# Performance work log

Hardware: AMD Instinct MI355X
Metric: run time of the kernel (lower is better)

Reference implementation:

```python
import jax, jax.numpy as jnp
import numpy as np

B, S_LEN, H, NH, NT, NL, I = 8, 2048, 768, 12, 32, 9, 3072
SPAN = 64
NSP = S_LEN // SPAN
TAG_RATE = 2
DH = H // NH
EPS = 1e-12


def rope(x):
    # interleaved-pair rotary position embedding, x: [B, L, H]
    L = x.shape[1]
    half = x.shape[2] // 2
    inv = 1.0 / (10000.0 ** (jnp.arange(half, dtype=jnp.float32) / half))
    ang = jnp.arange(L, dtype=jnp.float32)[:, None] * inv[None, :]  # [L, half]
    sin, cos = jnp.sin(ang), jnp.cos(ang)
    x2 = x.reshape(x.shape[0], L, half, 2)
    xe, xo = x2[..., 0], x2[..., 1]
    return jnp.stack([xe * cos - xo * sin, xe * sin + xo * cos], axis=-1).reshape(x.shape)


def layernorm(x, g, b):
    m = jnp.mean(x, axis=-1, keepdims=True)
    v = jnp.mean((x - m) ** 2, axis=-1, keepdims=True)
    return (x - m) * jax.lax.rsqrt(v + EPS) * g + b


def mha(q_in, kv_in, Wqkv, bqkv, Wo, bo):
    # torch nn.MultiheadAttention math (eval), batched over leading span axis
    Wq, Wk, Wv = jnp.split(Wqkv, 3, axis=0)
    bq, bk, bv = jnp.split(bqkv, 3)
    def heads(x, W, b):
        return (x @ W.T + b).reshape(x.shape[0], x.shape[1], NH, DH)
    q = heads(q_in, Wq, bq)
    k = heads(kv_in, Wk, bk)
    v = heads(kv_in, Wv, bv)
    scores = jnp.einsum('nqhd,nkhd->nhqk', q, k) * (1.0 / DH ** 0.5)
    a = jax.nn.softmax(scores, axis=-1)
    o = jnp.einsum('nhqk,nkhd->nqhd', a, v).reshape(q_in.shape[0], q_in.shape[1], H)
    return o @ Wo.T + bo


def setup_inputs() -> dict:
    key = jax.random.key(0)
    ks = jax.random.split(key, 16)
    p = lambda i, shape: (0.02 * jax.random.normal(ks[i], shape)).astype(jnp.float32)
    inp = {}
    inp['word_embedding'] = jax.random.normal(ks[0], (B, S_LEN, H), dtype=jnp.float32)
    # fixed-length, non-overlapping spans covering the sequence
    inp['span_starts'] = jnp.broadcast_to(jnp.arange(NSP, dtype=jnp.int32) * SPAN, (B, NSP))
    inp['span_tags'] = jax.random.randint(ks[1], (B, NSP), 0, NT)
    inp['tag_emb'] = p(2, (NT, H))
    inp['sa_Wqkv'] = p(3, (3 * H, H)); inp['sa_bqkv'] = jnp.zeros((3 * H,), jnp.float32)
    inp['sa_Wo'] = p(4, (H, H)); inp['sa_bo'] = jnp.zeros((H,), jnp.float32)
    inp['at_Wqkv'] = p(5, (3 * H, H)); inp['at_bqkv'] = jnp.zeros((3 * H,), jnp.float32)
    inp['at_Wo'] = p(6, (H, H)); inp['at_bo'] = jnp.zeros((H,), jnp.float32)
    inp['an_g'] = jnp.ones((H,), jnp.float32); inp['an_b'] = jnp.zeros((H,), jnp.float32)
    inp['W1'] = p(7, (I, H)); inp['b1'] = jnp.zeros((I,), jnp.float32)
    inp['W2'] = p(8, (H, I)); inp['b2'] = jnp.zeros((H,), jnp.float32)
    inp['fn_g'] = jnp.ones((H,), jnp.float32); inp['fn_b'] = jnp.zeros((H,), jnp.float32)
    inp['Wout'] = p(9, (NL, H)); inp['bout'] = jnp.zeros((NL,), jnp.float32)
    return inp


def reference(word_embedding, span_starts, span_tags, tag_emb,
              sa_Wqkv, sa_bqkv, sa_Wo, sa_bo,
              at_Wqkv, at_bqkv, at_Wo, at_bo,
              an_g, an_b, W1, b1, W2, b2, fn_g, fn_b, Wout, bout):
    raw = word_embedding  # hidden dropout p=0 (eval) -> identity
    xe = rope(word_embedding)
    # pack all spans: [B, NSP*SPAN] token positions
    pos = (span_starts[..., None] + jnp.arange(SPAN)).reshape(B, NSP * SPAN)
    spans = jnp.take_along_axis(xe, pos[..., None], axis=1).reshape(B * NSP, SPAN, H)
    # if_add_a_self_attention: X += self_attention(X, X, X)
    X = spans + mha(spans, spans, sa_Wqkv, sa_bqkv, sa_Wo, sa_bo)
    # enumerate_mode == 'self_attention': prepend tag embedding token, self-attend, drop it
    tagv = tag_emb[span_tags.reshape(-1)][:, None, :]  # [B*NSP, 1, H]
    qkv = jnp.concatenate([tagv, X], axis=1)           # [B*NSP, SPAN+1, H]
    res = mha(qkv, qkv, at_Wqkv, at_bqkv, at_Wo, at_bo)[:, 1:, :]
    # scatter-add results back into the full sequence
    taged = jnp.zeros_like(word_embedding).at[jnp.arange(B)[:, None], pos].add(
        res.reshape(B, NSP * SPAN, H))
    # if_merge_by_add branch
    out_emb = layernorm(raw + taged * TAG_RATE, an_g, an_b)
    ff = jax.nn.relu(out_emb @ W1.T + b1) @ W2.T + b2
    out = layernorm(ff + out_emb, fn_g, fn_b)
    return out @ Wout.T + bout
```

## Files before the change

### kernel.cpp

```cpp
#include <hip/hip_runtime.h>


typedef __attribute__((ext_vector_type(8))) short short8;
typedef __attribute__((ext_vector_type(4))) float f32x4;

typedef const __attribute__((address_space(1))) unsigned int* gas1_t;
typedef __attribute__((address_space(3))) unsigned int* las3_t;

#define DEVI static __device__ __forceinline__
#define VMCNT(n) asm volatile("s_waitcnt vmcnt(" #n ")" ::: "memory")

DEVI void gload_lds16(const void* g, void* l){
  __builtin_amdgcn_global_load_lds((gas1_t)g, (las3_t)l, 16, 0, 0);
}

DEVI unsigned short f2bf(float f){
  union { float f; unsigned u; } v; v.f = f;
  unsigned u = v.u;
  return (unsigned short)((u + 0x7fffu + ((u >> 16) & 1u)) >> 16);
}
DEVI float bf2f(unsigned short h){
  union { unsigned u; float f; } v; v.u = ((unsigned)h) << 16; return v.f;
}

__global__ void k_ropetab(float2* __restrict__ tab){
  int idx = blockIdx.x * 256 + threadIdx.x;
  if (idx >= 2048 * 384) return;
  int l = idx / 384, i = idx % 384;
  float inv = __expf(-(float)i * (9.210340371976184f / 384.0f));
  float ang = (float)l * inv;
  tab[idx] = make_float2(cosf(ang), sinf(ang));
}

__global__ void k_f2bf(const float* __restrict__ src, unsigned short* __restrict__ dst, int n){
  int i = blockIdx.x * 256 + threadIdx.x;
  if (i * 4 >= n) return;
  float4 v = *(const float4*)(src + (size_t)i * 4);
  ushort4 o;
  o.x = f2bf(v.x); o.y = f2bf(v.y); o.z = f2bf(v.z); o.w = f2bf(v.w);
  *(ushort4*)(dst + (size_t)i * 4) = o;
}

__global__ void k_gather_rope(const float* __restrict__ we, const int* __restrict__ starts,
                              const float2* __restrict__ tab, unsigned short* __restrict__ spans){
  int idx = blockIdx.x * 256 + threadIdx.x;
  int r  = idx / 192;
  int c4 = idx % 192;
  int span = r >> 6, s = r & 63;
  int b = span >> 5;
  int l = starts[span] + s;
  float4 x = *(const float4*)(we + ((size_t)b * 2048 + l) * 768 + c4 * 4);
  int i0 = c4 * 2;
  float2 cs0 = tab[l * 384 + i0];
  float2 cs1 = tab[l * 384 + i0 + 1];
  ushort4 o;
  o.x = f2bf(x.x * cs0.x - x.y * cs0.y);
  o.y = f2bf(x.x * cs0.y + x.y * cs0.x);
  o.z = f2bf(x.z * cs1.x - x.w * cs1.y);
  o.w = f2bf(x.z * cs1.y + x.w * cs1.x);
  *(ushort4*)(spans + (size_t)r * 768 + c4 * 4) = o;
}

__global__ void k_fill_tag(const float* __restrict__ tag_emb, const int* __restrict__ tags,
                           unsigned short* __restrict__ at_in){
  int span = blockIdx.x;
  int tag = tags[span];
  const float* src = tag_emb + (size_t)tag * 768;
  unsigned short* dst = at_in + (size_t)span * 65 * 768;
  for (int j = threadIdx.x; j < 768; j += 256) dst[j] = f2bf(src[j]);
}

template<int EPI>
__global__ __launch_bounds__(512, 2)
void k_gemm256(const unsigned short* __restrict__ A, const unsigned short* __restrict__ Bw,
               const float* __restrict__ bias, void* __restrict__ outp,
               const unsigned short* __restrict__ resid, int M, int N, int K, int nbx)
{
  __shared__ unsigned short Asl[4 * 256 * 32];
  __shared__ unsigned short Bsl[4 * 256 * 32];
  const int t0 = threadIdx.x;
  const int w = t0 >> 6, lane = t0 & 63;
  const int g = lane >> 4, li = lane & 15;
  const int wm = w >> 2, wn = w & 3;

  const int nwg = gridDim.x;
  const int bid = blockIdx.x;
  const int q = nwg >> 3, r8 = nwg & 7;
  const int xcd = bid & 7, off = bid >> 3;
  const int swz = (xcd < r8 ? xcd * (q + 1) : r8 * (q + 1) + (xcd - r8) * q) + off;
  const int m0 = (swz / nbx) * 256, n0 = (swz % nbx) * 256;

  const int srow = lane >> 2;
  const int sgc = (((lane & 3) ^ ((lane >> 3) & 3)) << 3);
  const int cs = ((g ^ ((li >> 1) & 3)) << 3);

  f32x4 acc[8][4];
  #pragma unroll
  for (int i = 0; i < 8; i++)
    #pragma unroll
    for (int j = 0; j < 4; j++) acc[i][j] = f32x4{0.f, 0.f, 0.f, 0.f};

  const int KT = K >> 5;

  #define STAGE(t_, s_) do { \
    const unsigned short* ga0 = A  + (size_t)(m0 +       w*16 + srow) * K + (t_)*32 + sgc; \
    const unsigned short* ga1 = A  + (size_t)(m0 + 128 + w*16 + srow) * K + (t_)*32 + sgc; \
    const unsigned short* gb0 = Bw + (size_t)(n0 +       w*16 + srow) * K + (t_)*32 + sgc; \
    const unsigned short* gb1 = Bw + (size_t)(n0 + 128 + w*16 + srow) * K + (t_)*32 + sgc; \
    gload_lds16(ga0, Asl + (s_)*8192 + (      w*16)*32); \
    gload_lds16(ga1, Asl + (s_)*8192 + (128 + w*16)*32); \
    gload_lds16(gb0, Bsl + (s_)*8192 + (      w*16)*32); \
    gload_lds16(gb1, Bsl + (s_)*8192 + (128 + w*16)*32); \
  } while(0)

  STAGE(0, 0);
  STAGE(1, 1);
  VMCNT(4);
  __builtin_amdgcn_s_barrier();

  for (int t = 0; t < KT; ++t){
    const int slot = t & 3;
    const unsigned short* As = Asl + slot * 8192;
    const unsigned short* Bs = Bsl + slot * 8192;

    short8 af[8], bfr[4];
    #pragma unroll
    for (int m = 0; m < 8; m++)
      af[m] = *(const short8*)(As + (wm * 128 + m * 16 + li) * 32 + cs);
    #pragma unroll
    for (int n = 0; n < 4; n++)
      bfr[n] = *(const short8*)(Bs + (wn * 64 + n * 16 + li) * 32 + cs);

    if (t + 2 < KT) STAGE(t + 2, (t + 2) & 3);

    #pragma unroll
    for (int m = 0; m < 8; m++)
      #pragma unroll
      for (int n = 0; n < 4; n++)
        acc[m][n] = __builtin_amdgcn_mfma_f32_16x16x32_bf16(af[m], bfr[n], acc[m][n], 0, 0, 0);

    if (t + 1 < KT){
      __builtin_amdgcn_sched_barrier(0);
      if (t + 2 < KT) { VMCNT(4); } else { VMCNT(0); }
      __builtin_amdgcn_s_barrier();
    }
  }
  #undef STAGE

  unsigned short* outb = (unsigned short*)outp;
  float* outf = (float*)outp;
  #pragma unroll
  for (int m = 0; m < 8; m++){
    const int row = m0 + wm * 128 + m * 16 + g * 4;
    #pragma unroll
    for (int n = 0; n < 4; n++){
      const int col = n0 + wn * 64 + n * 16 + li;
      const float bv = bias[col];
      #pragma unroll
      for (int r = 0; r < 4; r++){
        float v = acc[m][n][r] + bv;
        const int orow = row + r;
        if (EPI == 1) v += bf2f(resid[(size_t)orow * N + col]);
        if (EPI == 3) v = v > 0.f ? v : 0.f;
        if (EPI == 2){
          outf[(size_t)orow * N + col] = v;
        } else if (EPI == 1){
          outb[(size_t)(orow + orow / 64 + 1) * N + col] = f2bf(v);
        } else {
          outb[(size_t)orow * N + col] = f2bf(v);
        }
      }
    }
  }
}

template<int AT>
__global__ __launch_bounds__(64)
void k_attn(const unsigned short* __restrict__ qkv, unsigned short* __restrict__ outp)
{
  constexpr int Lkv  = AT ? 65 : 64;
  constexpr int qoff = AT ? 1 : 0;
  constexpr int NKF  = AT ? 5 : 4;
  constexpr int VK   = AT ? 65 : 64;
  constexpr int KKPV = AT ? 3 : 2;
  const int h = blockIdx.x;
  const int span = blockIdx.y;
  const int base = span * Lkv;
  const int lane = threadIdx.x;
  const int g = lane >> 4, li = lane & 15;

  __shared__ unsigned short P[64 * 104];
  if (AT){
    #pragma unroll
    for (int j = 0; j < 16; j++) P[lane * 104 + 80 + j] = 0;
  }

  short8 qf[4][2];
  #pragma unroll
  for (int m = 0; m < 4; m++)
    #pragma unroll
    for (int kq = 0; kq < 2; kq++)
      qf[m][kq] = *(const short8*)(qkv + (size_t)(base + qoff + m * 16 + li) * 2304 + h * 64 + kq * 32 + g * 8);

  f32x4 sc[4][NKF];
  #pragma unroll
  for (int m = 0; m < 4; m++)
    #pragma unroll
    for (int n = 0; n < NKF; n++) sc[m][n] = f32x4{0.f, 0.f, 0.f, 0.f};

  #pragma unroll
  for (int kq = 0; kq < 2; kq++){
    #pragma unroll
    for (int n = 0; n < NKF; n++){
      int krow = n * 16 + li; if (krow >= Lkv) krow = Lkv - 1;
      short8 kf = *(const short8*)(qkv + (size_t)(base + krow) * 2304 + 768 + h * 64 + kq * 32 + g * 8);
      #pragma unroll
      for (int m = 0; m < 4; m++)
        sc[m][n] = __builtin_amdgcn_mfma_f32_16x16x32_bf16(qf[m][kq], kf, sc[m][n], 0, 0, 0);
    }
  }

  const float scale = 0.125f;
  #pragma unroll
  for (int m = 0; m < 4; m++){
    #pragma unroll
    for (int r = 0; r < 4; r++){
      float mx = -1e30f;
      #pragma unroll
      for (int n = 0; n < NKF; n++){
        float v = sc[m][n][r] * scale;
        if (n * 16 + li >= VK) v = -1e30f;
        sc[m][n][r] = v;
        mx = fmaxf(mx, v);
      }
      mx = fmaxf(mx, __shfl_xor(mx, 1, 64));
      mx = fmaxf(mx, __shfl_xor(mx, 2, 64));
      mx = fmaxf(mx, __shfl_xor(mx, 4, 64));
      mx = fmaxf(mx, __shfl_xor(mx, 8, 64));
      float sum = 0.f;
      #pragma unroll
      for (int n = 0; n < NKF; n++){
        float p = __expf(sc[m][n][r] - mx);
        sc[m][n][r] = p;
        sum += p;
      }
      sum += __shfl_xor(sum, 1, 64);
      sum += __shfl_xor(sum, 2, 64);
      sum += __shfl_xor(sum, 4, 64);
      sum += __shfl_xor(sum, 8, 64);
      const float inv = 1.f / sum;
      const int prow = m * 16 + g * 4 + r;
      #pragma unroll
      for (int n = 0; n < NKF; n++)
        P[prow * 104 + n * 16 + li] = f2bf(sc[m][n][r] * inv);
    }
  }
  __syncthreads();

  f32x4 oacc[4][4];
  #pragma unroll
  for (int m = 0; m < 4; m++)
    #pragma unroll
    for (int n = 0; n < 4; n++) oacc[m][n] = f32x4{0.f, 0.f, 0.f, 0.f};

  #pragma unroll
  for (int kp = 0; kp < KKPV; kp++){
    short8 pf[4];
    #pragma unroll
    for (int m = 0; m < 4; m++)
      pf[m] = *(const short8*)(P + (m * 16 + li) * 104 + kp * 32 + g * 8);
    #pragma unroll
    for (int n = 0; n < 4; n++){
      short8 vf;
      #pragma unroll
      for (int i = 0; i < 8; i++){
        int k = kp * 32 + g * 8 + i;
        unsigned short vv = 0;
        if (k < VK) vv = qkv[(size_t)(base + k) * 2304 + 1536 + h * 64 + n * 16 + li];
        vf[i] = (short)vv;
      }
      #pragma unroll
      for (int m = 0; m < 4; m++)
        oacc[m][n] = __builtin_amdgcn_mfma_f32_16x16x32_bf16(pf[m], vf, oacc[m][n], 0, 0, 0);
    }
  }

  #pragma unroll
  for (int m = 0; m < 4; m++)
    #pragma unroll
    for (int n = 0; n < 4; n++)
      #pragma unroll
      for (int r = 0; r < 4; r++){
        int q = m * 16 + g * 4 + r;
        outp[(size_t)(span * 64 + q) * 768 + h * 64 + n * 16 + li] = f2bf(oacc[m][n][r]);
      }
}

__global__ __launch_bounds__(256)
void k_ln1(const float* __restrict__ raw, const float* __restrict__ res,
           const int* __restrict__ starts, const float* __restrict__ gg,
           const float* __restrict__ bb, unsigned short* __restrict__ oe16)
{
  int wave = threadIdx.x >> 6, lane = threadIdx.x & 63;
  int r = blockIdx.x * 4 + wave;
  int span = r >> 6, s = r & 63;
  int b = span >> 5;
  int l = starts[span] + s;
  const float* rp = raw + ((size_t)b * 2048 + l) * 768;
  const float* qp = res + (size_t)r * 768;
  float x[12];
  float sum = 0.f;
  #pragma unroll
  for (int j = 0; j < 12; j++){
    int c = lane + j * 64;
    x[j] = rp[c] + 2.f * qp[c];
    sum += x[j];
  }
  #pragma unroll
  for (int o = 1; o < 64; o <<= 1) sum += __shfl_xor(sum, o, 64);
  float mean = sum * (1.f / 768.f);
  float vs = 0.f;
  #pragma unroll
  for (int j = 0; j < 12; j++){ float d = x[j] - mean; vs += d * d; }
  #pragma unroll
  for (int o = 1; o < 64; o <<= 1) vs += __shfl_xor(vs, o, 64);
  float rstd = rsqrtf(vs * (1.f / 768.f) + 1e-12f);
  size_t ob = ((size_t)b * 2048 + l) * 768;
  #pragma unroll
  for (int j = 0; j < 12; j++){
    int c = lane + j * 64;
    float y = (x[j] - mean) * rstd * gg[c] + bb[c];
    oe16[ob + c] = f2bf(y);
  }
}

__global__ __launch_bounds__(256)
void k_ln2_out(const unsigned short* __restrict__ ff2, const unsigned short* __restrict__ oe,
               const float* __restrict__ gg, const float* __restrict__ bb,
               const float* __restrict__ Wout, const float* __restrict__ bout,
               float* __restrict__ out)
{
  int wave = threadIdx.x >> 6, lane = threadIdx.x & 63;
  int t = blockIdx.x * 4 + wave;
  const unsigned short* fp = ff2 + (size_t)t * 768;
  const unsigned short* ep = oe  + (size_t)t * 768;
  float x[12];
  float sum = 0.f;
  #pragma unroll
  for (int j = 0; j < 12; j++){
    int c = lane + j * 64;
    x[j] = bf2f(fp[c]) + bf2f(ep[c]);
    sum += x[j];
  }
  #pragma unroll
  for (int o = 1; o < 64; o <<= 1) sum += __shfl_xor(sum, o, 64);
  float mean = sum * (1.f / 768.f);
  float vs = 0.f;
  #pragma unroll
  for (int j = 0; j < 12; j++){ float d = x[j] - mean; vs += d * d; }
  #pragma unroll
  for (int o = 1; o < 64; o <<= 1) vs += __shfl_xor(vs, o, 64);
  float rstd = rsqrtf(vs * (1.f / 768.f) + 1e-12f);
  #pragma unroll
  for (int j = 0; j < 12; j++){
    int c = lane + j * 64;
    x[j] = (x[j] - mean) * rstd * gg[c] + bb[c];
  }
  for (int n = 0; n < 9; n++){
    float p = 0.f;
    #pragma unroll
    for (int j = 0; j < 12; j++){
      int c = lane + j * 64;
      p += x[j] * Wout[n * 768 + c];
    }
    #pragma unroll
    for (int o = 1; o < 64; o <<= 1) p += __shfl_xor(p, o, 64);
    if (lane == 0) out[(size_t)t * 9 + n] = p + bout[n];
  }
}

extern "C" void kernel_launch(void* const* d_in, const int* in_sizes, int n_in,
                              void* d_out, int out_size, void* d_ws, size_t ws_size,
                              hipStream_t stream)
{
  const float* we      = (const float*)d_in[0];
  const int*   starts  = (const int*)d_in[1];
  const int*   tags    = (const int*)d_in[2];
  const float* tag_emb = (const float*)d_in[3];
  const float* sa_Wqkv = (const float*)d_in[4];
  const float* sa_bqkv = (const float*)d_in[5];
  const float* sa_Wo   = (const float*)d_in[6];
  const float* sa_bo   = (const float*)d_in[7];
  const float* at_Wqkv = (const float*)d_in[8];
  const float* at_bqkv = (const float*)d_in[9];
  const float* at_Wo   = (const float*)d_in[10];
  const float* at_bo   = (const float*)d_in[11];
  const float* an_g    = (const float*)d_in[12];
  const float* an_b    = (const float*)d_in[13];
  const float* W1      = (const float*)d_in[14];
  const float* b1      = (const float*)d_in[15];
  const float* W2      = (const float*)d_in[16];
  const float* b2      = (const float*)d_in[17];
  const float* fn_g    = (const float*)d_in[18];
  const float* fn_b    = (const float*)d_in[19];
  const float* Wout    = (const float*)d_in[20];
  const float* bout    = (const float*)d_in[21];
  float* out = (float*)d_out;
  char* ws = (char*)d_ws;

  unsigned short* spans   = (unsigned short*)(ws + 0);
  unsigned short* at_in   = (unsigned short*)(ws + 25165824);
  unsigned short* attno   = (unsigned short*)(ws + 50724864);
  unsigned short* qkv     = (unsigned short*)(ws + 75890688);
  float2*         ropetab = (float2*)(ws + 75890688);
  float*          resf    = (float*)(ws + 75890688);
  unsigned short* oe16    = (unsigned short*)(ws + 0);
  unsigned short* ff1     = (unsigned short*)(ws + 25165824);
  unsigned short* ff2     = (unsigned short*)(ws + 125829120);
  unsigned short* wb      = (unsigned short*)(ws + 152567808);
  unsigned short* sa_Wqkv_b = wb;
  unsigned short* sa_Wo_b   = sa_Wqkv_b + 2304 * 768;
  unsigned short* at_Wqkv_b = sa_Wo_b   + 768 * 768;
  unsigned short* at_Wo_b   = at_Wqkv_b + 2304 * 768;
  unsigned short* W1_b      = at_Wo_b   + 768 * 768;
  unsigned short* W2_b      = W1_b      + 3072 * 768;

  k_ropetab<<<3072, 256, 0, stream>>>(ropetab);
  k_f2bf<<<1728, 256, 0, stream>>>(sa_Wqkv, sa_Wqkv_b, 2304 * 768);
  k_f2bf<<< 576, 256, 0, stream>>>(sa_Wo,   sa_Wo_b,    768 * 768);
  k_f2bf<<<1728, 256, 0, stream>>>(at_Wqkv, at_Wqkv_b, 2304 * 768);
  k_f2bf<<< 576, 256, 0, stream>>>(at_Wo,   at_Wo_b,    768 * 768);
  k_f2bf<<<2304, 256, 0, stream>>>(W1,      W1_b,      3072 * 768);
  k_f2bf<<<2304, 256, 0, stream>>>(W2,      W2_b,       768 * 3072);
  k_gather_rope<<<12288, 256, 0, stream>>>(we, starts, ropetab, spans);

  k_gemm256<0><<<576, 512, 0, stream>>>(spans, sa_Wqkv_b, sa_bqkv, qkv, nullptr, 16384, 2304, 768, 9);
  k_attn<0><<<dim3(12, 256), 64, 0, stream>>>(qkv, attno);
  k_fill_tag<<<256, 256, 0, stream>>>(tag_emb, tags, at_in);
  k_gemm256<1><<<192, 512, 0, stream>>>(attno, sa_Wo_b, sa_bo, at_in, spans, 16384, 768, 768, 3);
  k_gemm256<0><<<585, 512, 0, stream>>>(at_in, at_Wqkv_b, at_bqkv, qkv, nullptr, 16640, 2304, 768, 9);
  k_attn<1><<<dim3(12, 256), 64, 0, stream>>>(qkv, attno);
  k_gemm256<2><<<192, 512, 0, stream>>>(attno, at_Wo_b, at_bo, resf, nullptr, 16384, 768, 768, 3);
  k_ln1<<<4096, 256, 0, stream>>>(we, resf, starts, an_g, an_b, oe16);
  k_gemm256<3><<<768, 512, 0, stream>>>(oe16, W1_b, b1, ff1, nullptr, 16384, 3072, 768, 12);
  k_gemm256<0><<<192, 512, 0, stream>>>(ff1, W2_b, b2, ff2, nullptr, 16384, 768, 3072, 3);
  k_ln2_out<<<4096, 256, 0, stream>>>(ff2, oe16, fn_g, fn_b, Wout, bout, out);
}
```

Before: 500.6 us.

## Deepen GEMM prefetch to three stages, swizzle tiles, merge weight casts

The GEMM prefetch depth goes from two to three K-tiles in flight, using the fourth LDS slot, with vmcnt waits adjusted to match. MFMA sections are wrapped in s_setprio so math waves get issue priority. The block-to-tile mapping is reworked into 4x3 supertile groups, with a tail row for M=16640, to improve L2 reuse. The six weight-cast launches are merged into a single kernel. The costs are more outstanding loads per wave and a tile mapping that assumes nbx is divisible by 3.

```diff
diff --git a/kernel.cpp b/kernel.cpp
--- a/kernel.cpp
+++ b/kernel.cpp
@@ -8,10 +8,15 @@
 typedef __attribute__((address_space(3))) unsigned int* las3_t;
 
 #define DEVI static __device__ __forceinline__
-#define VMCNT(n) asm volatile("s_waitcnt vmcnt(" #n ")" ::: "memory")
 
 DEVI void gload_lds16(const void* g, void* l){
   __builtin_amdgcn_global_load_lds((gas1_t)g, (las3_t)l, 16, 0, 0);
+}
+
+template<int N> DEVI void vmcnt_imm(){
+  if constexpr (N == 8) asm volatile("s_waitcnt vmcnt(8)" ::: "memory");
+  else if constexpr (N == 4) asm volatile("s_waitcnt vmcnt(4)" ::: "memory");
+  else asm volatile("s_waitcnt vmcnt(0)" ::: "memory");
 }
 
 DEVI unsigned short f2bf(float f){
@@ -32,13 +37,23 @@
   tab[idx] = make_float2(cosf(ang), sinf(ang));
 }
 
-__global__ void k_f2bf(const float* __restrict__ src, unsigned short* __restrict__ dst, int n){
+__global__ void k_f2bf_all(const float* __restrict__ s0, const float* __restrict__ s1,
+                           const float* __restrict__ s2, const float* __restrict__ s3,
+                           const float* __restrict__ s4, const float* __restrict__ s5,
+                           unsigned short* __restrict__ dst){
   int i = blockIdx.x * 256 + threadIdx.x;
-  if (i * 4 >= n) return;
-  float4 v = *(const float4*)(src + (size_t)i * 4);
+  int e = i * 4;
+  const float* src; int off;
+  if      (e < 1769472){ src = s0; off = e; }
+  else if (e < 2359296){ src = s1; off = e - 1769472; }
+  else if (e < 4128768){ src = s2; off = e - 2359296; }
+  else if (e < 4718592){ src = s3; off = e - 4128768; }
+  else if (e < 7077888){ src = s4; off = e - 4718592; }
+  else                 { src = s5; off = e - 7077888; }
+  float4 v = *(const float4*)(src + off);
   ushort4 o;
   o.x = f2bf(v.x); o.y = f2bf(v.y); o.z = f2bf(v.z); o.w = f2bf(v.w);
-  *(ushort4*)(dst + (size_t)i * 4) = o;
+  *(ushort4*)(dst + e) = o;
 }
 
 __global__ void k_gather_rope(const float* __restrict__ we, const int* __restrict__ starts,
@@ -88,7 +103,16 @@
   const int q = nwg >> 3, r8 = nwg & 7;
   const int xcd = bid & 7, off = bid >> 3;
   const int swz = (xcd < r8 ? xcd * (q + 1) : r8 * (q + 1) + (xcd - r8) * q) + off;
-  const int m0 = (swz / nbx) * 256, n0 = (swz % nbx) * 256;
+  int mt, nt;
+  const int main_ = nbx << 6;
+  if (swz >= main_){ mt = 64; nt = swz - main_; }
+  else {
+    const int s = swz / 12, wv = swz % 12;
+    const int nsc = nbx / 3;
+    mt = (s / nsc) * 4 + (wv & 3);
+    nt = (s % nsc) * 3 + (wv >> 2);
+  }
+  const int m0 = mt * 256, n0 = nt * 256;
 
   const int srow = lane >> 2;
   const int sgc = (((lane & 3) ^ ((lane >> 3) & 3)) << 3);
@@ -115,7 +139,8 @@
 
   STAGE(0, 0);
   STAGE(1, 1);
-  VMCNT(4);
+  STAGE(2, 2);
+  vmcnt_imm<8>();
   __builtin_amdgcn_s_barrier();
 
   for (int t = 0; t < KT; ++t){
@@ -131,17 +156,21 @@
     for (int n = 0; n < 4; n++)
       bfr[n] = *(const short8*)(Bs + (wn * 64 + n * 16 + li) * 32 + cs);
 
-    if (t + 2 < KT) STAGE(t + 2, (t + 2) & 3);
-
+    if (t + 3 < KT) STAGE(t + 3, (t + 3) & 3);
+
+    __builtin_amdgcn_s_setprio(1);
     #pragma unroll
     for (int m = 0; m < 8; m++)
       #pragma unroll
       for (int n = 0; n < 4; n++)
         acc[m][n] = __builtin_amdgcn_mfma_f32_16x16x32_bf16(af[m], bfr[n], acc[m][n], 0, 0, 0);
+    __builtin_amdgcn_s_setprio(0);
 
     if (t + 1 < KT){
       __builtin_amdgcn_sched_barrier(0);
-      if (t + 2 < KT) { VMCNT(4); } else { VMCNT(0); }
+      if (t + 3 < KT)      vmcnt_imm<8>();
+      else if (t + 2 < KT) vmcnt_imm<4>();
+      else                 vmcnt_imm<0>();
       __builtin_amdgcn_s_barrier();
     }
   }
@@ -426,12 +455,7 @@
   unsigned short* W2_b      = W1_b      + 3072 * 768;
 
   k_ropetab<<<3072, 256, 0, stream>>>(ropetab);
-  k_f2bf<<<1728, 256, 0, stream>>>(sa_Wqkv, sa_Wqkv_b, 2304 * 768);
-  k_f2bf<<< 576, 256, 0, stream>>>(sa_Wo,   sa_Wo_b,    768 * 768);
-  k_f2bf<<<1728, 256, 0, stream>>>(at_Wqkv, at_Wqkv_b, 2304 * 768);
-  k_f2bf<<< 576, 256, 0, stream>>>(at_Wo,   at_Wo_b,    768 * 768);
-  k_f2bf<<<2304, 256, 0, stream>>>(W1,      W1_b,      3072 * 768);
-  k_f2bf<<<2304, 256, 0, stream>>>(W2,      W2_b,       768 * 3072);
+  k_f2bf_all<<<9216, 256, 0, stream>>>(sa_Wqkv, sa_Wo, at_Wqkv, at_Wo, W1, W2, wb);
   k_gather_rope<<<12288, 256, 0, stream>>>(we, starts, ropetab, spans);
 
   k_gemm256<0><<<576, 512, 0, stream>>>(spans, sa_Wqkv_b, sa_bqkv, qkv, nullptr, 16384, 2304, 768, 9);
```

Measured after the change: 500.0 us. No clear change (-0.1%).
